# Kernel optimization log

Measured on AMD Instinct MI355X. Metric: run time of the kernel, lower is better.

The kernel has to match this reference:

```python
import jax, jax.numpy as jnp
import numpy as np

N_NODES = 50000
N_EDGES = 600000
IN_CH = 64
HID = 128
N_GRAPHS = 64
EPS = 0.0  # GINEConv default eps


def setup_inputs() -> dict:
    key = jax.random.key(0)
    ks = jax.random.split(key, 16)
    x = jax.random.normal(ks[0], (N_NODES, IN_CH), dtype=jnp.float32)
    edge_index = jax.random.randint(ks[1], (2, N_EDGES), 0, N_NODES, dtype=jnp.int64)
    edge_attr = jax.random.normal(ks[2], (N_EDGES, 3), dtype=jnp.float32)
    batch = jnp.sort(jax.random.randint(ks[3], (N_NODES,), 0, N_GRAPHS, dtype=jnp.int64))
    s = lambda fan_in: 1.0 / np.sqrt(fan_in)
    # conv1: edge lin (3->IN_CH), mlp (IN_CH->HID->HID)
    el1_w = jax.random.uniform(ks[4], (3, IN_CH), minval=-s(3), maxval=s(3))
    el1_b = jnp.zeros((IN_CH,), jnp.float32)
    w1a = jax.random.uniform(ks[5], (IN_CH, HID), minval=-s(IN_CH), maxval=s(IN_CH))
    b1a = jnp.zeros((HID,), jnp.float32)
    w1b = jax.random.uniform(ks[6], (HID, HID), minval=-s(HID), maxval=s(HID))
    b1b = jnp.zeros((HID,), jnp.float32)
    # conv2: edge lin (3->HID), mlp (HID->HID->HID)
    el2_w = jax.random.uniform(ks[7], (3, HID), minval=-s(3), maxval=s(3))
    el2_b = jnp.zeros((HID,), jnp.float32)
    w2a = jax.random.uniform(ks[8], (HID, HID), minval=-s(HID), maxval=s(HID))
    b2a = jnp.zeros((HID,), jnp.float32)
    w2b = jax.random.uniform(ks[9], (HID, HID), minval=-s(HID), maxval=s(HID))
    b2b = jnp.zeros((HID,), jnp.float32)
    return dict(x=x, edge_index=edge_index, edge_attr=edge_attr, batch=batch,
                el1_w=el1_w, el1_b=el1_b, w1a=w1a, b1a=b1a, w1b=w1b, b1b=b1b,
                el2_w=el2_w, el2_b=el2_b, w2a=w2a, b2a=b2a, w2b=w2b, b2b=b2b)


def _gine_conv(x, src, dst, edge_attr, el_w, el_b, wa, ba, wb, bb):
    # message: relu(x_j + Lin(edge_attr)), aggregated (sum) at target nodes
    e = edge_attr @ el_w + el_b              # [E, d]
    msg = jax.nn.relu(x[src] + e)            # [E, d]
    agg = jax.ops.segment_sum(msg, dst, num_segments=x.shape[0])  # [N, d]
    h = (1.0 + EPS) * x + agg
    h = jax.nn.relu(h @ wa + ba) @ wb + bb   # MLP
    return h


def reference(x, edge_index, edge_attr, batch,
              el1_w, el1_b, w1a, b1a, w1b, b1b,
              el2_w, el2_b, w2a, b2a, w2b, b2b):
    src, dst = edge_index[0], edge_index[1]
    h = jax.nn.relu(_gine_conv(x, src, dst, edge_attr, el1_w, el1_b, w1a, b1a, w1b, b1b))
    h = jax.nn.relu(_gine_conv(h, src, dst, edge_attr, el2_w, el2_b, w2a, b2a, w2b, b2b))
    # global mean pool per graph
    sums = jax.ops.segment_sum(h, batch, num_segments=N_GRAPHS)
    cnt = jax.ops.segment_sum(jnp.ones((h.shape[0],), h.dtype), batch, num_segments=N_GRAPHS)
    return sums / jnp.maximum(cnt, 1.0)[:, None]
```

## Files before the change

kernel.cpp:

```cpp
#include <hip/hip_runtime.h>

#define N_NODES 50000
#define N_EDGES 600000
#define N_PAD 50048
#define IN_CH 64
#define HID 128
#define N_GRAPHS 64
#define SCAN_BLOCKS 196

typedef __attribute__((ext_vector_type(8))) short bf16x8;
typedef __attribute__((ext_vector_type(4))) float f32x4;

__device__ __forceinline__ float bf2f(unsigned short u) {
    union { unsigned int i; float f; } v; v.i = ((unsigned int)u) << 16; return v.f;
}
__device__ __forceinline__ unsigned short f2bf(float f) {
    union { float f; unsigned int i; } v; v.f = f;
    unsigned int u = v.i;
    return (unsigned short)((u + 0x7FFFu + ((u >> 16) & 1u)) >> 16);
}

__global__ void prep_kernel(const float* __restrict__ w1a, const float* __restrict__ w1b,
                            const float* __restrict__ w2a, const float* __restrict__ w2b,
                            unsigned short* __restrict__ waT1, unsigned short* __restrict__ wbT1,
                            unsigned short* __restrict__ waT2, unsigned short* __restrict__ wbT2,
                            int* __restrict__ deg, float* __restrict__ psum) {
    int i = blockIdx.x * blockDim.x + threadIdx.x;
    if (i < N_NODES) deg[i] = 0;
    if (i < N_GRAPHS * HID) psum[i] = 0.f;
    if (i < IN_CH * HID) {
        int k = i / HID, n = i % HID;
        waT1[n * IN_CH + k] = f2bf(w1a[i]);
    }
    if (i < HID * HID) {
        int k = i / HID, n = i % HID;
        wbT1[n * HID + k] = f2bf(w1b[i]);
        waT2[n * HID + k] = f2bf(w2a[i]);
        wbT2[n * HID + k] = f2bf(w2b[i]);
    }
}

__global__ void hist_kernel(const int* __restrict__ ei, int* __restrict__ deg) {
    int base = (blockIdx.x * blockDim.x + threadIdx.x) * 4;
    if (base < N_EDGES) {
        int4 d = *(const int4*)(ei + N_EDGES + base);
        atomicAdd(&deg[d.x], 1);
        atomicAdd(&deg[d.y], 1);
        atomicAdd(&deg[d.z], 1);
        atomicAdd(&deg[d.w], 1);
    }
}

__device__ __forceinline__ int block_incl_scan256(int v, int* sm, int t) {
    int val = v;
    sm[t] = val; __syncthreads();
    #pragma unroll
    for (int off = 1; off < 256; off <<= 1) {
        int n = (t >= off) ? sm[t - off] : 0;
        __syncthreads();
        val += n; sm[t] = val; __syncthreads();
    }
    return val;
}

__global__ void scan1_kernel(const int* __restrict__ deg, int* __restrict__ partials) {
    __shared__ int sm[256];
    int t = threadIdx.x;
    int i = blockIdx.x * 256 + t;
    int v = (i < N_NODES) ? deg[i] : 0;
    sm[t] = v; __syncthreads();
    for (int off = 128; off > 0; off >>= 1) {
        if (t < off) sm[t] += sm[t + off];
        __syncthreads();
    }
    if (t == 0) partials[blockIdx.x] = sm[0];
}

__global__ void scan2_kernel(int* __restrict__ partials) {
    __shared__ int sm[256];
    int t = threadIdx.x;
    int v = (t < SCAN_BLOCKS) ? partials[t] : 0;
    int incl = block_incl_scan256(v, sm, t);
    if (t < SCAN_BLOCKS) partials[t] = incl - v;
}

__global__ void scan3_kernel(const int* __restrict__ deg,
                             const int* __restrict__ partials,
                             int* __restrict__ rowptr,
                             int* __restrict__ cursor) {
    __shared__ int sm[256];
    int t = threadIdx.x;
    int i = blockIdx.x * 256 + t;
    int v = (i < N_NODES) ? deg[i] : 0;
    int incl = block_incl_scan256(v, sm, t);
    int excl = incl - v + partials[blockIdx.x];
    if (i < N_NODES) { rowptr[i] = excl; cursor[i] = excl; }
    if (blockIdx.x == 0 && t == 0) rowptr[N_NODES] = N_EDGES;
}

__global__ void scatter_kernel(const int* __restrict__ ei,
                               const float* __restrict__ ea,
                               int* __restrict__ cursor,
                               int4* __restrict__ edata) {
    int base = (blockIdx.x * blockDim.x + threadIdx.x) * 4;
    if (base >= N_EDGES) return;
    int4 s = *(const int4*)(ei + base);
    int4 d = *(const int4*)(ei + N_EDGES + base);
    const float4* ea4 = (const float4*)(ea + (size_t)base * 3);
    float4 A = ea4[0], B = ea4[1], C = ea4[2];
    int p0 = atomicAdd(&cursor[d.x], 1);
    int p1 = atomicAdd(&cursor[d.y], 1);
    int p2 = atomicAdd(&cursor[d.z], 1);
    int p3 = atomicAdd(&cursor[d.w], 1);
    edata[p0] = make_int4(s.x, __float_as_int(A.x), __float_as_int(A.y), __float_as_int(A.z));
    edata[p1] = make_int4(s.y, __float_as_int(A.w), __float_as_int(B.x), __float_as_int(B.y));
    edata[p2] = make_int4(s.z, __float_as_int(B.z), __float_as_int(B.w), __float_as_int(C.x));
    edata[p3] = make_int4(s.w, __float_as_int(C.y), __float_as_int(C.z), __float_as_int(C.w));
}

__global__ void gather64_kernel(const float* __restrict__ xin,
                                const int4* __restrict__ edata,
                                const int* __restrict__ rowptr,
                                const float* __restrict__ elw,
                                const float* __restrict__ elb,
                                unsigned short* __restrict__ sg) {
    constexpr int K = IN_CH;
    constexpr int NPB = 8;
    const int node0 = blockIdx.x * NPB;
    const int t = threadIdx.x;
    const int c = t & 63, half = t >> 6;
    const float w0 = elw[c], w1 = elw[K + c], w2 = elw[2 * K + c], eb = elb[c];

    auto term = [&](int4 e, float row) -> float {
        float ev = __int_as_float(e.y) * w0 + __int_as_float(e.z) * w1 +
                   __int_as_float(e.w) * w2 + eb;
        float m = row + ev;
        return m > 0.f ? m : 0.f;
    };

    for (int i = 0; i < NPB; i += 2) {
        int node = node0 + i + half;
        float acc = xin[(size_t)node * K + c];
        int jb = rowptr[node], je = rowptr[node + 1];
        int j = jb;
        for (; j + 8 <= je; j += 8) {
            int4 e0 = edata[j],     e1 = edata[j + 1], e2 = edata[j + 2], e3 = edata[j + 3];
            int4 e4 = edata[j + 4], e5 = edata[j + 5], e6 = edata[j + 6], e7 = edata[j + 7];
            float r0 = xin[(size_t)e0.x * K + c];
            float r1 = xin[(size_t)e1.x * K + c];
            float r2 = xin[(size_t)e2.x * K + c];
            float r3 = xin[(size_t)e3.x * K + c];
            float r4 = xin[(size_t)e4.x * K + c];
            float r5 = xin[(size_t)e5.x * K + c];
            float r6 = xin[(size_t)e6.x * K + c];
            float r7 = xin[(size_t)e7.x * K + c];
            acc += term(e0, r0) + term(e1, r1) + term(e2, r2) + term(e3, r3)
                 + term(e4, r4) + term(e5, r5) + term(e6, r6) + term(e7, r7);
        }
        for (; j + 4 <= je; j += 4) {
            int4 e0 = edata[j], e1 = edata[j + 1], e2 = edata[j + 2], e3 = edata[j + 3];
            float r0 = xin[(size_t)e0.x * K + c];
            float r1 = xin[(size_t)e1.x * K + c];
            float r2 = xin[(size_t)e2.x * K + c];
            float r3 = xin[(size_t)e3.x * K + c];
            acc += term(e0, r0) + term(e1, r1) + term(e2, r2) + term(e3, r3);
        }
        for (; j < je; j++) {
            int4 e0 = edata[j];
            acc += term(e0, xin[(size_t)e0.x * K + c]);
        }
        sg[(size_t)node * K + c] = f2bf(acc);
    }
}

__global__ void gather128_kernel(const unsigned short* __restrict__ xin,
                                 const int4* __restrict__ edata,
                                 const int* __restrict__ rowptr,
                                 const float* __restrict__ elw,
                                 const float* __restrict__ elb,
                                 unsigned short* __restrict__ sg) {
    constexpr int NPW = 4;
    const int t = threadIdx.x;
    const int w = t >> 6, l = t & 63;
    const unsigned* x32 = (const unsigned*)xin;
    unsigned* sg32 = (unsigned*)sg;
    const int c0 = 2 * l;
    const float w00 = elw[c0],           w01 = elw[c0 + 1];
    const float w10 = elw[HID + c0],     w11 = elw[HID + c0 + 1];
    const float w20 = elw[2 * HID + c0], w21 = elw[2 * HID + c0 + 1];
    const float eb0 = elb[c0],           eb1 = elb[c0 + 1];
    const int node0 = (blockIdx.x * 4 + w) * NPW;

    for (int ni = 0; ni < NPW; ni++) {
        int node = node0 + ni;
        unsigned sv = x32[(size_t)node * 64 + l];
        float acc0 = bf2f((unsigned short)(sv & 0xFFFF));
        float acc1 = bf2f((unsigned short)(sv >> 16));
        auto term2 = [&](int4 e, unsigned r) {
            float A0 = __int_as_float(e.y), A1 = __int_as_float(e.z), A2 = __int_as_float(e.w);
            float ev0 = A0 * w00 + A1 * w10 + A2 * w20 + eb0;
            float ev1 = A0 * w01 + A1 * w11 + A2 * w21 + eb1;
            float m0 = bf2f((unsigned short)(r & 0xFFFF)) + ev0;
            float m1 = bf2f((unsigned short)(r >> 16)) + ev1;
            acc0 += m0 > 0.f ? m0 : 0.f;
            acc1 += m1 > 0.f ? m1 : 0.f;
        };
        int jb = rowptr[node], je = rowptr[node + 1];
        int j = jb;
        for (; j + 8 <= je; j += 8) {
            int4 e0 = edata[j],     e1 = edata[j + 1], e2 = edata[j + 2], e3 = edata[j + 3];
            int4 e4 = edata[j + 4], e5 = edata[j + 5], e6 = edata[j + 6], e7 = edata[j + 7];
            unsigned r0 = x32[(size_t)e0.x * 64 + l];
            unsigned r1 = x32[(size_t)e1.x * 64 + l];
            unsigned r2 = x32[(size_t)e2.x * 64 + l];
            unsigned r3 = x32[(size_t)e3.x * 64 + l];
            unsigned r4 = x32[(size_t)e4.x * 64 + l];
            unsigned r5 = x32[(size_t)e5.x * 64 + l];
            unsigned r6 = x32[(size_t)e6.x * 64 + l];
            unsigned r7 = x32[(size_t)e7.x * 64 + l];
            term2(e0, r0); term2(e1, r1); term2(e2, r2); term2(e3, r3);
            term2(e4, r4); term2(e5, r5); term2(e6, r6); term2(e7, r7);
        }
        for (; j + 4 <= je; j += 4) {
            int4 e0 = edata[j], e1 = edata[j + 1], e2 = edata[j + 2], e3 = edata[j + 3];
            unsigned r0 = x32[(size_t)e0.x * 64 + l];
            unsigned r1 = x32[(size_t)e1.x * 64 + l];
            unsigned r2 = x32[(size_t)e2.x * 64 + l];
            unsigned r3 = x32[(size_t)e3.x * 64 + l];
            term2(e0, r0); term2(e1, r1); term2(e2, r2); term2(e3, r3);
        }
        for (; j < je; j++) {
            int4 e0 = edata[j];
            term2(e0, x32[(size_t)e0.x * 64 + l]);
        }
        sg32[(size_t)node * 64 + l] = (unsigned)f2bf(acc0) | ((unsigned)f2bf(acc1) << 16);
    }
}

template <int K, bool POOL>
__global__ __launch_bounds__(256)
void mlp_mfma_kernel(const unsigned short* __restrict__ sg,
                     const unsigned short* __restrict__ waT,
                     const float* __restrict__ ba,
                     const unsigned short* __restrict__ wbT,
                     const float* __restrict__ bb,
                     void* __restrict__ outv,
                     const int* __restrict__ batch) {
    constexpr int HSTR = 136;
    constexpr int OSTR = HID + 4;
    __shared__ __align__(16) unsigned short sHid[4][16 * HSTR];
    __shared__ __align__(16) float sOut[64 * OSTR];
    const int t = threadIdx.x;
    const int w = t >> 6, l = t & 63;
    const int i16 = l & 15, q = l >> 4;
    const int blk0 = blockIdx.x * 64;
    const int row0 = blk0 + w * 16;

    bf16x8 aA[K / 32];
    #pragma unroll
    for (int s = 0; s < K / 32; s++)
        aA[s] = *(const bf16x8*)&sg[(size_t)(row0 + i16) * K + s * 32 + q * 8];
    unsigned short* myHid = sHid[w];
    #pragma unroll
    for (int ct = 0; ct < 8; ct++) {
        int col = ct * 16 + i16;
        float bv = ba[col];
        f32x4 acc = (f32x4){bv, bv, bv, bv};
        #pragma unroll
        for (int s = 0; s < K / 32; s++) {
            bf16x8 b = *(const bf16x8*)&waT[(size_t)col * K + s * 32 + q * 8];
            acc = __builtin_amdgcn_mfma_f32_16x16x32_bf16(aA[s], b, acc, 0, 0, 0);
        }
        #pragma unroll
        for (int r = 0; r < 4; r++) {
            float v = acc[r] > 0.f ? acc[r] : 0.f;
            myHid[(q * 4 + r) * HSTR + col] = f2bf(v);
        }
    }
    __syncthreads();

    bf16x8 aB[4];
    #pragma unroll
    for (int s = 0; s < 4; s++)
        aB[s] = *(const bf16x8*)&myHid[i16 * HSTR + s * 32 + q * 8];
    #pragma unroll
    for (int ct = 0; ct < 8; ct++) {
        int col = ct * 16 + i16;
        float bv = bb[col];
        f32x4 acc = (f32x4){bv, bv, bv, bv};
        #pragma unroll
        for (int s = 0; s < 4; s++) {
            bf16x8 b = *(const bf16x8*)&wbT[(size_t)col * HID + s * 32 + q * 8];
            acc = __builtin_amdgcn_mfma_f32_16x16x32_bf16(aB[s], b, acc, 0, 0, 0);
        }
        #pragma unroll
        for (int r = 0; r < 4; r++) {
            float v = acc[r] > 0.f ? acc[r] : 0.f;
            sOut[(w * 16 + q * 4 + r) * OSTR + col] = v;
        }
    }
    __syncthreads();

    if (POOL) {
        if (t < HID) {
            float* psum = (float*)outv;
            float acc = 0.f;
            int curg = batch[blk0];
            for (int row = 0; row < 64; row++) {
                int node = blk0 + row;
                if (node >= N_NODES) break;
                int g = batch[node];
                if (g != curg) {
                    atomicAdd(&psum[curg * HID + t], acc);
                    acc = 0.f; curg = g;
                }
                acc += sOut[row * OSTR + t];
            }
            atomicAdd(&psum[curg * HID + t], acc);
        }
    } else {
        unsigned short* hout = (unsigned short*)outv;
        for (int idx = t; idx < 64 * 16; idx += 256) {
            int row = idx >> 4, ch = idx & 15;
            int node = blk0 + row;
            if (node < N_NODES) {
                float4 f0 = *(const float4*)&sOut[row * OSTR + ch * 8];
                float4 f1 = *(const float4*)&sOut[row * OSTR + ch * 8 + 4];
                uint4 u;
                u.x = (unsigned)f2bf(f0.x) | ((unsigned)f2bf(f0.y) << 16);
                u.y = (unsigned)f2bf(f0.z) | ((unsigned)f2bf(f0.w) << 16);
                u.z = (unsigned)f2bf(f1.x) | ((unsigned)f2bf(f1.y) << 16);
                u.w = (unsigned)f2bf(f1.z) | ((unsigned)f2bf(f1.w) << 16);
                *(uint4*)&hout[(size_t)node * HID + ch * 8] = u;
            }
        }
    }
}

__global__ void pool_div_kernel(const float* __restrict__ sums,
                                const int* __restrict__ batch,
                                float* __restrict__ out) {
    int i = blockIdx.x * blockDim.x + threadIdx.x;
    if (i >= N_GRAPHS * HID) return;
    int g = i / HID;
    int lo = 0, hi = N_NODES;
    while (lo < hi) { int mid = (lo + hi) >> 1; if (batch[mid] < g) lo = mid + 1; else hi = mid; }
    int start = lo;
    lo = 0; hi = N_NODES;
    while (lo < hi) { int mid = (lo + hi) >> 1; if (batch[mid] <= g) lo = mid + 1; else hi = mid; }
    float c = (float)(lo - start);
    out[i] = sums[i] / (c > 1.0f ? c : 1.0f);
}

extern "C" void kernel_launch(void* const* d_in, const int* in_sizes, int n_in,
                              void* d_out, int out_size, void* d_ws, size_t ws_size,
                              hipStream_t stream) {
    const float* x    = (const float*)d_in[0];
    const int*   ei   = (const int*)d_in[1];
    const float* ea   = (const float*)d_in[2];
    const int*   batch= (const int*)d_in[3];
    const float* el1w = (const float*)d_in[4];
    const float* el1b = (const float*)d_in[5];
    const float* w1a  = (const float*)d_in[6];
    const float* b1a  = (const float*)d_in[7];
    const float* w1b  = (const float*)d_in[8];
    const float* b1b  = (const float*)d_in[9];
    const float* el2w = (const float*)d_in[10];
    const float* el2b = (const float*)d_in[11];
    const float* w2a  = (const float*)d_in[12];
    const float* b2a  = (const float*)d_in[13];
    const float* w2b  = (const float*)d_in[14];
    const float* b2b  = (const float*)d_in[15];
    float* out = (float*)d_out;

    int4*  edata    = (int4*)d_ws;
    float* psum     = (float*)(edata + N_EDGES);
    int*   deg      = (int*)(psum + N_GRAPHS * HID);
    int*   cursor   = deg + N_NODES;
    int*   rowptr   = cursor + N_NODES;
    int*   partials = rowptr + N_NODES + 1;
    unsigned short* hbf  = (unsigned short*)((char*)psum + (size_t)158452 * 4);
    unsigned short* sgbuf= hbf + (size_t)N_NODES * HID;
    unsigned short* waT1 = sgbuf + (size_t)N_PAD * HID;
    unsigned short* wbT1 = waT1 + HID * IN_CH;
    unsigned short* waT2 = wbT1 + HID * HID;
    unsigned short* wbT2 = waT2 + HID * HID;

    prep_kernel<<<(N_NODES + 255) / 256, 256, 0, stream>>>(
        w1a, w1b, w2a, w2b, waT1, wbT1, waT2, wbT2, deg, psum);
    hist_kernel<<<(N_EDGES / 4 + 255) / 256, 256, 0, stream>>>(ei, deg);
    scan1_kernel<<<SCAN_BLOCKS, 256, 0, stream>>>(deg, partials);
    scan2_kernel<<<1, 256, 0, stream>>>(partials);
    scan3_kernel<<<SCAN_BLOCKS, 256, 0, stream>>>(deg, partials, rowptr, cursor);
    scatter_kernel<<<(N_EDGES / 4 + 255) / 256, 256, 0, stream>>>(ei, ea, cursor, edata);

    gather64_kernel<<<N_NODES / 8, 128, 0, stream>>>(
        x, edata, rowptr, el1w, el1b, sgbuf);
    mlp_mfma_kernel<IN_CH, false><<<N_PAD / 64, 256, 0, stream>>>(
        sgbuf, waT1, b1a, wbT1, b1b, hbf, nullptr);

    gather128_kernel<<<N_NODES / 16, 256, 0, stream>>>(
        hbf, edata, rowptr, el2w, el2b, sgbuf);
    mlp_mfma_kernel<HID, true><<<N_PAD / 64, 256, 0, stream>>>(
        sgbuf, waT2, b2a, wbT2, b2b, psum, batch);

    pool_div_kernel<<<(N_GRAPHS * HID + 255) / 256, 256, 0, stream>>>(psum, batch, out);
}
```

Measured before the change: 306.8 us.

## Pack edge records to 8 bytes and interleave two nodes in gather128

Each CSR edge record shrinks from an int4 to a uint2. The source index now sits in the low 16 bits, and the three edge attributes are stored as bf16. This halves edge-record traffic in the scatter and in both gather kernels. gather128 also processes two nodes together so that more independent row loads are in flight per wave. The costs are bf16 rounding of edge attributes and a hard limit of fewer than 65536 nodes on the source index.

```diff
diff --git a/kernel.cpp b/kernel.cpp
--- a/kernel.cpp
+++ b/kernel.cpp
@@ -19,6 +19,7 @@
     unsigned int u = v.i;
     return (unsigned short)((u + 0x7FFFu + ((u >> 16) & 1u)) >> 16);
 }
+
 
 __global__ void prep_kernel(const float* __restrict__ w1a, const float* __restrict__ w1b,
                             const float* __restrict__ w2a, const float* __restrict__ w2b,
@@ -101,7 +102,7 @@
 __global__ void scatter_kernel(const int* __restrict__ ei,
                                const float* __restrict__ ea,
                                int* __restrict__ cursor,
-                               int4* __restrict__ edata) {
+                               uint2* __restrict__ edata) {
     int base = (blockIdx.x * blockDim.x + threadIdx.x) * 4;
     if (base >= N_EDGES) return;
     int4 s = *(const int4*)(ei + base);
@@ -112,14 +113,18 @@
     int p1 = atomicAdd(&cursor[d.y], 1);
     int p2 = atomicAdd(&cursor[d.z], 1);
     int p3 = atomicAdd(&cursor[d.w], 1);
-    edata[p0] = make_int4(s.x, __float_as_int(A.x), __float_as_int(A.y), __float_as_int(A.z));
-    edata[p1] = make_int4(s.y, __float_as_int(A.w), __float_as_int(B.x), __float_as_int(B.y));
-    edata[p2] = make_int4(s.z, __float_as_int(B.z), __float_as_int(B.w), __float_as_int(C.x));
-    edata[p3] = make_int4(s.w, __float_as_int(C.y), __float_as_int(C.z), __float_as_int(C.w));
+    edata[p0] = make_uint2((unsigned)s.x | ((unsigned)f2bf(A.x) << 16),
+                           (unsigned)f2bf(A.y) | ((unsigned)f2bf(A.z) << 16));
+    edata[p1] = make_uint2((unsigned)s.y | ((unsigned)f2bf(A.w) << 16),
+                           (unsigned)f2bf(B.x) | ((unsigned)f2bf(B.y) << 16));
+    edata[p2] = make_uint2((unsigned)s.z | ((unsigned)f2bf(B.z) << 16),
+                           (unsigned)f2bf(B.w) | ((unsigned)f2bf(C.x) << 16));
+    edata[p3] = make_uint2((unsigned)s.w | ((unsigned)f2bf(C.y) << 16),
+                           (unsigned)f2bf(C.z) | ((unsigned)f2bf(C.w) << 16));
 }
 
 __global__ void gather64_kernel(const float* __restrict__ xin,
-                                const int4* __restrict__ edata,
+                                const uint2* __restrict__ edata,
                                 const int* __restrict__ rowptr,
                                 const float* __restrict__ elw,
                                 const float* __restrict__ elb,
@@ -131,9 +136,10 @@
     const int c = t & 63, half = t >> 6;
     const float w0 = elw[c], w1 = elw[K + c], w2 = elw[2 * K + c], eb = elb[c];
 
-    auto term = [&](int4 e, float row) -> float {
-        float ev = __int_as_float(e.y) * w0 + __int_as_float(e.z) * w1 +
-                   __int_as_float(e.w) * w2 + eb;
+    auto term = [&](uint2 e, float row) -> float {
+        float ev = bf2f((unsigned short)(e.x >> 16)) * w0 +
+                   bf2f((unsigned short)(e.y & 0xFFFF)) * w1 +
+                   bf2f((unsigned short)(e.y >> 16)) * w2 + eb;
         float m = row + ev;
         return m > 0.f ? m : 0.f;
     };
@@ -144,42 +150,41 @@
         int jb = rowptr[node], je = rowptr[node + 1];
         int j = jb;
         for (; j + 8 <= je; j += 8) {
-            int4 e0 = edata[j],     e1 = edata[j + 1], e2 = edata[j + 2], e3 = edata[j + 3];
-            int4 e4 = edata[j + 4], e5 = edata[j + 5], e6 = edata[j + 6], e7 = edata[j + 7];
-            float r0 = xin[(size_t)e0.x * K + c];
-            float r1 = xin[(size_t)e1.x * K + c];
-            float r2 = xin[(size_t)e2.x * K + c];
-            float r3 = xin[(size_t)e3.x * K + c];
-            float r4 = xin[(size_t)e4.x * K + c];
-            float r5 = xin[(size_t)e5.x * K + c];
-            float r6 = xin[(size_t)e6.x * K + c];
-            float r7 = xin[(size_t)e7.x * K + c];
+            uint2 e0 = edata[j],     e1 = edata[j + 1], e2 = edata[j + 2], e3 = edata[j + 3];
+            uint2 e4 = edata[j + 4], e5 = edata[j + 5], e6 = edata[j + 6], e7 = edata[j + 7];
+            float r0 = xin[(size_t)(e0.x & 0xFFFF) * K + c];
+            float r1 = xin[(size_t)(e1.x & 0xFFFF) * K + c];
+            float r2 = xin[(size_t)(e2.x & 0xFFFF) * K + c];
+            float r3 = xin[(size_t)(e3.x & 0xFFFF) * K + c];
+            float r4 = xin[(size_t)(e4.x & 0xFFFF) * K + c];
+            float r5 = xin[(size_t)(e5.x & 0xFFFF) * K + c];
+            float r6 = xin[(size_t)(e6.x & 0xFFFF) * K + c];
+            float r7 = xin[(size_t)(e7.x & 0xFFFF) * K + c];
             acc += term(e0, r0) + term(e1, r1) + term(e2, r2) + term(e3, r3)
                  + term(e4, r4) + term(e5, r5) + term(e6, r6) + term(e7, r7);
         }
         for (; j + 4 <= je; j += 4) {
-            int4 e0 = edata[j], e1 = edata[j + 1], e2 = edata[j + 2], e3 = edata[j + 3];
-            float r0 = xin[(size_t)e0.x * K + c];
-            float r1 = xin[(size_t)e1.x * K + c];
-            float r2 = xin[(size_t)e2.x * K + c];
-            float r3 = xin[(size_t)e3.x * K + c];
+            uint2 e0 = edata[j], e1 = edata[j + 1], e2 = edata[j + 2], e3 = edata[j + 3];
+            float r0 = xin[(size_t)(e0.x & 0xFFFF) * K + c];
+            float r1 = xin[(size_t)(e1.x & 0xFFFF) * K + c];
+            float r2 = xin[(size_t)(e2.x & 0xFFFF) * K + c];
+            float r3 = xin[(size_t)(e3.x & 0xFFFF) * K + c];
             acc += term(e0, r0) + term(e1, r1) + term(e2, r2) + term(e3, r3);
         }
         for (; j < je; j++) {
-            int4 e0 = edata[j];
-            acc += term(e0, xin[(size_t)e0.x * K + c]);
+            uint2 e0 = edata[j];
+            acc += term(e0, xin[(size_t)(e0.x & 0xFFFF) * K + c]);
         }
         sg[(size_t)node * K + c] = f2bf(acc);
     }
 }
 
 __global__ void gather128_kernel(const unsigned short* __restrict__ xin,
-                                 const int4* __restrict__ edata,
+                                 const uint2* __restrict__ edata,
                                  const int* __restrict__ rowptr,
                                  const float* __restrict__ elw,
                                  const float* __restrict__ elb,
                                  unsigned short* __restrict__ sg) {
-    constexpr int NPW = 4;
     const int t = threadIdx.x;
     const int w = t >> 6, l = t & 63;
     const unsigned* x32 = (const unsigned*)xin;
@@ -189,51 +194,76 @@
     const float w10 = elw[HID + c0],     w11 = elw[HID + c0 + 1];
     const float w20 = elw[2 * HID + c0], w21 = elw[2 * HID + c0 + 1];
     const float eb0 = elb[c0],           eb1 = elb[c0 + 1];
-    const int node0 = (blockIdx.x * 4 + w) * NPW;
-
-    for (int ni = 0; ni < NPW; ni++) {
-        int node = node0 + ni;
-        unsigned sv = x32[(size_t)node * 64 + l];
-        float acc0 = bf2f((unsigned short)(sv & 0xFFFF));
-        float acc1 = bf2f((unsigned short)(sv >> 16));
-        auto term2 = [&](int4 e, unsigned r) {
-            float A0 = __int_as_float(e.y), A1 = __int_as_float(e.z), A2 = __int_as_float(e.w);
+    const int node0 = (blockIdx.x * 4 + w) * 4;
+
+    for (int ni = 0; ni < 4; ni += 2) {
+        int nA = node0 + ni, nB = node0 + ni + 1;
+        unsigned svA = x32[(size_t)nA * 64 + l];
+        unsigned svB = x32[(size_t)nB * 64 + l];
+        float a0 = bf2f((unsigned short)(svA & 0xFFFF));
+        float a1 = bf2f((unsigned short)(svA >> 16));
+        float b0 = bf2f((unsigned short)(svB & 0xFFFF));
+        float b1 = bf2f((unsigned short)(svB >> 16));
+
+        auto term2 = [&](uint2 e, unsigned r, float& p0, float& p1) {
+            float A0 = bf2f((unsigned short)(e.x >> 16));
+            float A1 = bf2f((unsigned short)(e.y & 0xFFFF));
+            float A2 = bf2f((unsigned short)(e.y >> 16));
             float ev0 = A0 * w00 + A1 * w10 + A2 * w20 + eb0;
             float ev1 = A0 * w01 + A1 * w11 + A2 * w21 + eb1;
             float m0 = bf2f((unsigned short)(r & 0xFFFF)) + ev0;
             float m1 = bf2f((unsigned short)(r >> 16)) + ev1;
-            acc0 += m0 > 0.f ? m0 : 0.f;
-            acc1 += m1 > 0.f ? m1 : 0.f;
+            p0 += m0 > 0.f ? m0 : 0.f;
+            p1 += m1 > 0.f ? m1 : 0.f;
         };
-        int jb = rowptr[node], je = rowptr[node + 1];
-        int j = jb;
-        for (; j + 8 <= je; j += 8) {
-            int4 e0 = edata[j],     e1 = edata[j + 1], e2 = edata[j + 2], e3 = edata[j + 3];
-            int4 e4 = edata[j + 4], e5 = edata[j + 5], e6 = edata[j + 6], e7 = edata[j + 7];
-            unsigned r0 = x32[(size_t)e0.x * 64 + l];
-            unsigned r1 = x32[(size_t)e1.x * 64 + l];
-            unsigned r2 = x32[(size_t)e2.x * 64 + l];
-            unsigned r3 = x32[(size_t)e3.x * 64 + l];
-            unsigned r4 = x32[(size_t)e4.x * 64 + l];
-            unsigned r5 = x32[(size_t)e5.x * 64 + l];
-            unsigned r6 = x32[(size_t)e6.x * 64 + l];
-            unsigned r7 = x32[(size_t)e7.x * 64 + l];
-            term2(e0, r0); term2(e1, r1); term2(e2, r2); term2(e3, r3);
-            term2(e4, r4); term2(e5, r5); term2(e6, r6); term2(e7, r7);
-        }
-        for (; j + 4 <= je; j += 4) {
-            int4 e0 = edata[j], e1 = edata[j + 1], e2 = edata[j + 2], e3 = edata[j + 3];
-            unsigned r0 = x32[(size_t)e0.x * 64 + l];
-            unsigned r1 = x32[(size_t)e1.x * 64 + l];
-            unsigned r2 = x32[(size_t)e2.x * 64 + l];
-            unsigned r3 = x32[(size_t)e3.x * 64 + l];
-            term2(e0, r0); term2(e1, r1); term2(e2, r2); term2(e3, r3);
-        }
-        for (; j < je; j++) {
-            int4 e0 = edata[j];
-            term2(e0, x32[(size_t)e0.x * 64 + l]);
-        }
-        sg32[(size_t)node * 64 + l] = (unsigned)f2bf(acc0) | ((unsigned)f2bf(acc1) << 16);
+
+        int ja = rowptr[nA], jaE = rowptr[nA + 1];
+        int jb = rowptr[nB], jbE = rowptr[nB + 1];
+        while (ja + 4 <= jaE && jb + 4 <= jbE) {
+            uint2 eA0 = edata[ja],     eA1 = edata[ja + 1], eA2 = edata[ja + 2], eA3 = edata[ja + 3];
+            uint2 eB0 = edata[jb],     eB1 = edata[jb + 1], eB2 = edata[jb + 2], eB3 = edata[jb + 3];
+            unsigned rA0 = x32[(size_t)(eA0.x & 0xFFFF) * 64 + l];
+            unsigned rA1 = x32[(size_t)(eA1.x & 0xFFFF) * 64 + l];
+            unsigned rA2 = x32[(size_t)(eA2.x & 0xFFFF) * 64 + l];
+            unsigned rA3 = x32[(size_t)(eA3.x & 0xFFFF) * 64 + l];
+            unsigned rB0 = x32[(size_t)(eB0.x & 0xFFFF) * 64 + l];
+            unsigned rB1 = x32[(size_t)(eB1.x & 0xFFFF) * 64 + l];
+            unsigned rB2 = x32[(size_t)(eB2.x & 0xFFFF) * 64 + l];
+            unsigned rB3 = x32[(size_t)(eB3.x & 0xFFFF) * 64 + l];
+            term2(eA0, rA0, a0, a1); term2(eA1, rA1, a0, a1);
+            term2(eA2, rA2, a0, a1); term2(eA3, rA3, a0, a1);
+            term2(eB0, rB0, b0, b1); term2(eB1, rB1, b0, b1);
+            term2(eB2, rB2, b0, b1); term2(eB3, rB3, b0, b1);
+            ja += 4; jb += 4;
+        }
+        for (; ja + 4 <= jaE; ja += 4) {
+            uint2 e0 = edata[ja], e1 = edata[ja + 1], e2 = edata[ja + 2], e3 = edata[ja + 3];
+            unsigned r0 = x32[(size_t)(e0.x & 0xFFFF) * 64 + l];
+            unsigned r1 = x32[(size_t)(e1.x & 0xFFFF) * 64 + l];
+            unsigned r2 = x32[(size_t)(e2.x & 0xFFFF) * 64 + l];
+            unsigned r3 = x32[(size_t)(e3.x & 0xFFFF) * 64 + l];
+            term2(e0, r0, a0, a1); term2(e1, r1, a0, a1);
+            term2(e2, r2, a0, a1); term2(e3, r3, a0, a1);
+        }
+        for (; ja < jaE; ja++) {
+            uint2 e0 = edata[ja];
+            term2(e0, x32[(size_t)(e0.x & 0xFFFF) * 64 + l], a0, a1);
+        }
+        for (; jb + 4 <= jbE; jb += 4) {
+            uint2 e0 = edata[jb], e1 = edata[jb + 1], e2 = edata[jb + 2], e3 = edata[jb + 3];
+            unsigned r0 = x32[(size_t)(e0.x & 0xFFFF) * 64 + l];
+            unsigned r1 = x32[(size_t)(e1.x & 0xFFFF) * 64 + l];
+            unsigned r2 = x32[(size_t)(e2.x & 0xFFFF) * 64 + l];
+            unsigned r3 = x32[(size_t)(e3.x & 0xFFFF) * 64 + l];
+            term2(e0, r0, b0, b1); term2(e1, r1, b0, b1);
+            term2(e2, r2, b0, b1); term2(e3, r3, b0, b1);
+        }
+        for (; jb < jbE; jb++) {
+            uint2 e0 = edata[jb];
+            term2(e0, x32[(size_t)(e0.x & 0xFFFF) * 64 + l], b0, b1);
+        }
+        sg32[(size_t)nA * 64 + l] = (unsigned)f2bf(a0) | ((unsigned)f2bf(a1) << 16);
+        sg32[(size_t)nB * 64 + l] = (unsigned)f2bf(b0) | ((unsigned)f2bf(b1) << 16);
     }
 }
 
@@ -373,7 +403,7 @@
     const float* b2b  = (const float*)d_in[15];
     float* out = (float*)d_out;
 
-    int4*  edata    = (int4*)d_ws;
+    uint2* edata    = (uint2*)d_ws;
     float* psum     = (float*)(edata + N_EDGES);
     int*   deg      = (int*)(psum + N_GRAPHS * HID);
     int*   cursor   = deg + N_NODES;
```

New measurement: 299.0 us. -2.5%, faster.
